# Performance work log

Hardware: AMD Instinct MI355X
Metric: run time of the kernel (lower is better)

## Reference

```python
import jax, jax.numpy as jnp
import numpy as np

NEG_INF = -1e30  # log-semiring zero
B, T, D, V, L = 16, 800, 512, 5000, 100


def setup_inputs() -> dict:
    key = jax.random.key(0)
    k1, k2, k3, k4, k5, k6 = jax.random.split(key, 6)
    hs_pad = jax.random.normal(k1, (B, T, D), dtype=jnp.float32)
    W = jax.random.normal(k2, (D, V), dtype=jnp.float32) / np.sqrt(D)
    b = jnp.zeros((V,), dtype=jnp.float32)
    hlens = jax.random.randint(k3, (B,), T // 2, T + 1, dtype=jnp.int32)
    labels = jax.random.randint(k4, (B, L), 1, V, dtype=jnp.int32)  # blank=0 excluded
    label_lens = jax.random.randint(k5, (B,), L // 2, L + 1, dtype=jnp.int32)
    return {"hs_pad": hs_pad, "W": W, "b": b, "hlens": hlens,
            "labels": labels, "label_lens": label_lens}


def _ctc_tot_scores(log_probs, hlens, labels, label_lens):
    # Standard CTC log-semiring forward DP (equivalent to k2 CTC-topology
    # intersect_dense + get_tot_scores). log_probs: [B,T,V], blank id = 0.
    Bb, Tt, Vv = log_probs.shape
    Ll = labels.shape[1]
    S = 2 * Ll + 1  # extended sequence: blank, l1, blank, l2, ..., blank
    ext = jnp.zeros((Bb, S), dtype=labels.dtype).at[:, 1::2].set(labels)
    # skip transition (s-2 -> s) allowed iff ext[s] != blank and ext[s] != ext[s-2]
    skip = jnp.concatenate(
        [jnp.zeros((Bb, 2), dtype=bool),
         (ext[:, 2:] != ext[:, :-2]) & (ext[:, 2:] != 0)], axis=1)
    # emissions along extended labels: lp_ext[b,t,s] = log_probs[b,t,ext[b,s]]
    lp_ext = jax.vmap(lambda lp, e: lp[:, e])(log_probs, ext)  # [B,T,S]
    alpha = jnp.full((Bb, S), NEG_INF, dtype=log_probs.dtype)
    alpha = alpha.at[:, 0].set(lp_ext[:, 0, 0])
    alpha = alpha.at[:, 1].set(lp_ext[:, 0, 1])

    def step(alpha, inp):
        t, lp_t = inp  # lp_t: [B,S]
        prev1 = jnp.pad(alpha[:, :-1], ((0, 0), (1, 0)), constant_values=NEG_INF)
        prev2 = jnp.pad(alpha[:, :-2], ((0, 0), (2, 0)), constant_values=NEG_INF)
        prev2 = jnp.where(skip, prev2, NEG_INF)
        a = jnp.logaddexp(jnp.logaddexp(alpha, prev1), prev2) + lp_t
        # freeze rows whose sequence has ended (t >= hlen)
        return jnp.where((t < hlens)[:, None], a, alpha), None

    ts = jnp.arange(1, Tt)
    alpha, _ = jax.lax.scan(step, alpha, (ts, jnp.swapaxes(lp_ext, 0, 1)[1:]))
    last = 2 * label_lens  # index of final blank per utterance
    a_last = jnp.take_along_axis(alpha, last[:, None], axis=1)[:, 0]
    a_prev = jnp.take_along_axis(alpha, (last - 1)[:, None], axis=1)[:, 0]
    return jnp.logaddexp(a_last, a_prev)  # [B] total log-likelihoods


def reference(hs_pad, W, b, hlens, labels, label_lens):
    # ctc_lo Linear (dropout_rate=0 -> identity) + log_softmax
    logits = jnp.einsum('btd,dv->btv', hs_pad, W) + b
    log_probs = jax.nn.log_softmax(logits, axis=-1)
    tot = _ctc_tot_scores(log_probs, hlens, labels, label_lens)
    # forward_scores = -tot_scores, reduce=True -> mean
    return jnp.mean(-tot)
```

## Files before the change

### kernel.cpp

```cpp
#include <hip/hip_runtime.h>

#define NEG_INF -1e30f

typedef __attribute__((ext_vector_type(8))) __bf16 bf16x8;
typedef __attribute__((ext_vector_type(4))) float f32x4;

constexpr int Bb = 16, T = 800, D = 512, V = 5000, L = 100;
constexpr int ROWS = Bb * T;
constexpr int S = 2 * L + 1;
constexpr int SP = 208;
constexpr int VP = 5120;
constexpr int NCB = VP / 128;
constexpr int NRB = ROWS / 128;
constexpr int NGB = Bb * 50;
constexpr int CONVB = ROWS * D / 1024;
constexpr int RSTRIDE = SP * 4;
constexpr int CH = 16;
constexpr int CHB = CH * RSTRIDE;

static __device__ __forceinline__ unsigned short f2bf(float x) {
  union { float f; unsigned u; } v; v.f = x;
  unsigned r = (v.u + 0x7FFFu + ((v.u >> 16) & 1u)) >> 16;
  return (unsigned short)r;
}

static __device__ __forceinline__ double dpp_shr1_zero_d(double x) {
  long long b = __double_as_longlong(x);
  int lo = (int)(b & 0xFFFFFFFFLL);
  int hi = (int)(b >> 32);
  int nlo = __builtin_amdgcn_update_dpp(0, lo, 0x138, 0xF, 0xF, false);
  int nhi = __builtin_amdgcn_update_dpp(0, hi, 0x138, 0xF, 0xF, false);
  return __longlong_as_double(((long long)(unsigned)nlo) | ((long long)nhi << 32));
}
static __device__ __forceinline__ double dpp_shl1_zero_d(double x) {
  long long b = __double_as_longlong(x);
  int lo = (int)(b & 0xFFFFFFFFLL);
  int hi = (int)(b >> 32);
  int nlo = __builtin_amdgcn_update_dpp(0, lo, 0x130, 0xF, 0xF, false);
  int nhi = __builtin_amdgcn_update_dpp(0, hi, 0x130, 0xF, 0xF, false);
  return __longlong_as_double(((long long)(unsigned)nlo) | ((long long)nhi << 32));
}
static __device__ __forceinline__ float dpp_shl1_zero_f(float x) {
  return __int_as_float(__builtin_amdgcn_update_dpp(
      0, __float_as_int(x), 0x130, 0xF, 0xF, false));
}

static __device__ __forceinline__ float ex2(float x) { return __builtin_amdgcn_exp2f(x); }
static __device__ __forceinline__ float lg2(float x) { return __builtin_amdgcn_logf(x); }

static __device__ __forceinline__ float lg2d(double z) {
  long long b = __double_as_longlong(z);
  int e = (int)((b >> 52) & 0x7FF);
  if (e == 0) return -1.0e30f;
  unsigned mant = (unsigned)((b >> 29) & 0x7FFFFFu);
  float mf = __int_as_float(0x3F800000u | mant);
  return (float)(e - 1023) + lg2(mf);
}

__global__ __launch_bounds__(256) void k_prep(const float* __restrict__ hs,
                                              const float* __restrict__ W,
                                              unsigned short* __restrict__ A,
                                              unsigned short* __restrict__ Wt) {
  __shared__ float tile[64][65];
  int blk = blockIdx.x;
  if (blk < CONVB) {
    int i = blk * 256 + threadIdx.x;
    float4 f = ((const float4*)hs)[i];
    ushort4 o;
    o.x = f2bf(f.x); o.y = f2bf(f.y); o.z = f2bf(f.z); o.w = f2bf(f.w);
    ((ushort4*)A)[i] = o;
    return;
  }
  int g = blk - CONVB;
  int v0 = (g % (VP / 64)) * 64, k0 = (g / (VP / 64)) * 64;
  int tl = threadIdx.x & 63, th = threadIdx.x >> 6;
#pragma unroll
  for (int i = 0; i < 16; i++) {
    int k = k0 + th + i * 4;
    int v = v0 + tl;
    tile[th + i * 4][tl] = (v < V) ? W[(size_t)k * V + v] : 0.f;
  }
  __syncthreads();
#pragma unroll
  for (int i = 0; i < 16; i++) {
    int v = v0 + th + i * 4;
    int k = k0 + tl;
    Wt[(size_t)v * D + k] = f2bf(tile[tl][th + i * 4]);
  }
}

__global__ __launch_bounds__(256) void k_gather(const unsigned short* __restrict__ A,
                                                const unsigned short* __restrict__ Wt,
                                                const float* __restrict__ bias,
                                                const int* __restrict__ labels,
                                                float* __restrict__ glog) {
  int tid = threadIdx.x;
  int lane = tid & 63, w = tid >> 6;
  int q = lane >> 4, c = lane & 15;
  int b = blockIdx.x & 15, chk = blockIdx.x >> 4;
  int t0 = chk * 16;
  int bT = b * T, bL = b * L;
  int st0 = (w == 0) ? 0 : 4 + (w - 1) * 3;
  int nst = (w == 0) ? 4 : 3;

  int evs[4]; float bvs[4];
#pragma unroll
  for (int j = 0; j < 4; j++) {
    int st = st0 + (j < nst ? j : nst - 1);
    int s = st * 16 + c;
    evs[j] = (s < S && (s & 1)) ? labels[bL + (s >> 1)] : 0;
    bvs[j] = bias[evs[j]];
  }
  const unsigned short* Arow = A + (size_t)(bT + t0 + c) * D;
  f32x4 acc[4];
#pragma unroll
  for (int j = 0; j < 4; j++) acc[j] = (f32x4){0.f, 0.f, 0.f, 0.f};
  for (int kk = 0; kk < D; kk += 32) {
    bf16x8 aa = *(const bf16x8*)(Arow + kk + q * 8);
#pragma unroll
    for (int j = 0; j < 4; j++) {
      bf16x8 bb = *(const bf16x8*)(Wt + (size_t)evs[j] * D + kk + q * 8);
      acc[j] = __builtin_amdgcn_mfma_f32_16x16x32_bf16(aa, bb, acc[j], 0, 0, 0);
    }
  }
#pragma unroll
  for (int j = 0; j < 4; j++) {
    if (j >= nst) break;
    int st = st0 + j;
#pragma unroll
    for (int r = 0; r < 4; r++)
      glog[(size_t)(bT + t0 + q * 4 + r) * SP + st * 16 + c] = acc[j][r] + bvs[j];
  }
}

#define RENORM4(A0, A1, A2, A3, KC) {                                           \
    long long ba0 = __double_as_longlong(A0), ba1 = __double_as_longlong(A1);   \
    long long ba2 = __double_as_longlong(A2), ba3 = __double_as_longlong(A3);   \
    int ee0 = (int)((ba0 >> 52) & 0x7FF), ee1 = (int)((ba1 >> 52) & 0x7FF);     \
    int ee2 = (int)((ba2 >> 52) & 0x7FF), ee3 = (int)((ba3 >> 52) & 0x7FF);     \
    int em = ee0 > ee1 ? ee0 : ee1;                                             \
    em = em > ee2 ? em : ee2;                                                   \
    em = em > ee3 ? em : ee3;                                                   \
    _Pragma("unroll")                                                           \
    for (int o = 1; o < 64; o <<= 1) { int q2 = __shfl_xor(em, o); em = em > q2 ? em : q2; } \
    if (em > 0 && em < 2046) {                                                  \
      double sc = __longlong_as_double((long long)(2046 - em) << 52);           \
      A0 *= sc; A1 *= sc; A2 *= sc; A3 *= sc;                                   \
      KC += em - 1023;                                                          \
    } }

__global__ __launch_bounds__(256) void k_fused(const unsigned short* __restrict__ A,
                                               const unsigned short* __restrict__ Wt,
                                               const float* __restrict__ bias,
                                               const float* __restrict__ glog,
                                               const int* __restrict__ labels,
                                               const int* __restrict__ hlens,
                                               const int* __restrict__ llens,
                                               float* __restrict__ partM,
                                               float* __restrict__ partS,
                                               float* __restrict__ rawtot) {
  __shared__ __attribute__((aligned(16))) char smem[65536];

  int blk = blockIdx.x;
  if (blk < Bb) {
    int tid = threadIdx.x;
    int w = tid >> 6, l = tid & 63;
    if (w >= 2) { __syncthreads(); return; }

    int b = blk;
    int col4 = ((4 * l < SP) ? 4 * l : SP - 4) * 4;
    const char* gvb = (const char*)glog + (size_t)b * T * RSTRIDE;
    int hl = hlens[b];
    int mfw = (hl - 1) >> 1;
    const size_t gmax = (size_t)T * RSTRIDE - 16;

    int i0 = (2 * l < L) ? 2 * l : L - 1;
    int i1 = (2 * l + 1 < L) ? 2 * l + 1 : L - 1;
    int im = (l >= 1) ? 2 * l - 1 : 0; im = im < L ? im : L - 1;
    int lab0 = labels[b * L + i0];
    int lab1 = labels[b * L + i1];
    int labm = labels[b * L + im];
    bool sk1 = (l >= 1) && (lab0 != 0) && (lab0 != labm);
    bool sk3 = (lab1 != 0) && (lab1 != lab0);

    constexpr float LOG2E = 1.44269504f;
    float* laf = (float*)(smem + 53248);
    float* lbf = (float*)(smem + 54080);

    if (w == 0) {
      f32x4 g0 = *(const f32x4*)(gvb + col4);
      double z0 = (l == 0) ? 1.0 : 0.0;
      double z1 = (l == 0) ? (double)ex2((g0.y - g0.x) * LOG2E) : 0.0;
      double z2 = 0.0, z3 = 0.0;
      double Csum = (double)g0.x;
      int Kc = 0;

      auto stageF = [&](int cc, int dst) {
        size_t sb = (size_t)(1 + cc * CH) * RSTRIDE;
#pragma unroll
        for (int pg = 0; pg < 13; pg++) {
          size_t ob = sb + (size_t)pg * 1024 + (size_t)l * 16;
          if (ob > gmax) ob = gmax;
          __builtin_amdgcn_global_load_lds(
              (const __attribute__((address_space(1))) void*)(gvb + ob),
              (__attribute__((address_space(3))) void*)(smem + dst * CHB + pg * 1024),
              16, 0, 0);
        }
      };

#define FW_STEPZ(G) {                                                  \
    float e1f = ex2(((G).y - (G).x) * LOG2E);                          \
    float e3f = ex2(((G).w - (G).x) * LOG2E);                          \
    Csum += (double)(G).x;                                             \
    double p3 = dpp_shr1_zero_d(z3);                                   \
    double nz0 = z0 + p3;                                              \
    double nz1 = (z1 + z0 + (sk1 ? p3 : 0.0)) * (double)e1f;           \
    double nz2 = z2 + z1;                                              \
    double nz3 = (z3 + z2 + (sk3 ? z1 : 0.0)) * (double)e3f;           \
    z0 = nz0; z1 = nz1; z2 = nz2; z3 = nz3; }

      int nchF = (mfw + CH - 1) / CH;
      stageF(0, 0);
      stageF(1, 1);
      for (int c = 0; c < nchF; ++c) {
        int cur = c & 1;
        if (c + 2 < nchF) { asm volatile("s_waitcnt vmcnt(13)" ::: "memory"); }
        else             { asm volatile("s_waitcnt vmcnt(0)" ::: "memory"); }
        __builtin_amdgcn_sched_barrier(0);
        const char* bufc = smem + cur * CHB + col4;
        int steps = mfw - c * CH; if (steps > CH) steps = CH;
        if (steps == CH) {
          f32x4 G[8];
#pragma unroll
          for (int j = 0; j < 8; j++) G[j] = *(const f32x4*)(bufc + j * RSTRIDE);
#pragma unroll
          for (int j = 0; j < 8; j++) FW_STEPZ(G[j])
#pragma unroll
          for (int j = 0; j < 8; j++) G[j] = *(const f32x4*)(bufc + (8 + j) * RSTRIDE);
#pragma unroll
          for (int j = 0; j < 8; j++) FW_STEPZ(G[j])
          RENORM4(z0, z1, z2, z3, Kc)
        } else {
          for (int j = 0; j < steps; j++) {
            f32x4 G = *(const f32x4*)(bufc + j * RSTRIDE);
            FW_STEPZ(G)
          }
        }
        if (c + 2 < nchF) {
          asm volatile("s_waitcnt lgkmcnt(0)" ::: "memory");
          stageF(c + 2, cur);
        }
      }
#undef FW_STEPZ
      if (l < 52) {
        float base = (float)(Csum * 1.4426950408889634 + (double)Kc);
        laf[4 * l + 0] = base + lg2d(z0);
        laf[4 * l + 1] = base + lg2d(z1);
        laf[4 * l + 2] = base + lg2d(z2);
        laf[4 * l + 3] = base + lg2d(z3);
      }
    } else {
      int ll = llens[b];
      int sA = 2 * ll, sB = sA - 1;
      int s0i = 4 * l;
      double b0 = (s0i == sA || s0i == sB) ? 1.0 : 0.0;
      double b1 = (s0i + 1 == sA || s0i + 1 == sB) ? 1.0 : 0.0;
      double b2 = (s0i + 2 == sA || s0i + 2 == sB) ? 1.0 : 0.0;
      double b3 = (s0i + 3 == sA || s0i + 3 == sB) ? 1.0 : 0.0;
      double Csum = 0.0;
      int Kc = 0;
      int sk1i = sk1 ? 1 : 0;
      bool sk1n = __shfl_down(sk1i, 1) != 0;

      auto stageB = [&](int cc, int dst) {
        int rlo = hl - 1 - cc * CH - 15;
        size_t sb = (size_t)rlo * RSTRIDE;
#pragma unroll
        for (int pg = 0; pg < 13; pg++) {
          size_t ob = sb + (size_t)pg * 1024 + (size_t)l * 16;
          if (ob > gmax) ob = gmax;
          __builtin_amdgcn_global_load_lds(
              (const __attribute__((address_space(1))) void*)(gvb + ob),
              (__attribute__((address_space(3))) void*)(smem + dst * CHB + pg * 1024),
              16, 0, 0);
        }
      };

#define BW_STEPZ(G) {                                                  \
    float e1f = ex2(((G).y - (G).x) * LOG2E);                          \
    float e3f = ex2(((G).w - (G).x) * LOG2E);                          \
    float e1s = dpp_shl1_zero_f(e1f);                                  \
    Csum += (double)(G).x;                                             \
    double b1s = dpp_shl1_zero_d(b1);                                  \
    double q4  = dpp_shl1_zero_d(b0);                                  \
    double f1 = b1 * (double)e1f;                                      \
    double f3 = b3 * (double)e3f;                                      \
    double q5 = b1s * (double)e1s;                                     \
    double nb0 = b0 + f1;                                              \
    double nb1 = f1 + b2 + (sk3 ? f3 : 0.0);                           \
    double nb2 = b2 + f3;                                              \
    double nb3 = f3 + q4 + (sk1n ? q5 : 0.0);                          \
    b0 = nb0; b1 = nb1; b2 = nb2; b3 = nb3; }

      int bsteps = (hl - 1) - mfw;
      int nchB = (bsteps + CH - 1) / CH;
      stageB(0, 2);
      stageB(1, 3);
      for (int c = 0; c < nchB; ++c) {
        int cur = c & 1;
        if (c + 2 < nchB) { asm volatile("s_waitcnt vmcnt(13)" ::: "memory"); }
        else             { asm volatile("s_waitcnt vmcnt(0)" ::: "memory"); }
        __builtin_amdgcn_sched_barrier(0);
        const char* bufc = smem + (2 + cur) * CHB + col4;
        int hi = hl - 1 - c * CH;
        int steps = hi - mfw; if (steps > CH) steps = CH;
        if (steps == CH) {
          f32x4 G[8];
#pragma unroll
          for (int j = 0; j < 8; j++) G[j] = *(const f32x4*)(bufc + (15 - j) * RSTRIDE);
#pragma unroll
          for (int j = 0; j < 8; j++) BW_STEPZ(G[j])
#pragma unroll
          for (int j = 0; j < 8; j++) G[j] = *(const f32x4*)(bufc + (7 - j) * RSTRIDE);
#pragma unroll
          for (int j = 0; j < 8; j++) BW_STEPZ(G[j])
          RENORM4(b0, b1, b2, b3, Kc)
        } else {
          for (int j = 0; j < steps; j++) {
            f32x4 G = *(const f32x4*)(bufc + (15 - j) * RSTRIDE);
            BW_STEPZ(G)
          }
        }
        if (c + 2 < nchB) {
          asm volatile("s_waitcnt lgkmcnt(0)" ::: "memory");
          stageB(c + 2, 2 + cur);
        }
      }
#undef BW_STEPZ
      if (l < 52) {
        float base = (float)(Csum * 1.4426950408889634 + (double)Kc);
        lbf[4 * l + 0] = base + lg2d(b0);
        lbf[4 * l + 1] = base + lg2d(b1);
        lbf[4 * l + 2] = base + lg2d(b2);
        lbf[4 * l + 3] = base + lg2d(b3);
      }
    }

    __syncthreads();
    if (w == 0) {
      float v[4];
#pragma unroll
      for (int r = 0; r < 4; r++) {
        int s = 4 * l + r;
        v[r] = (l < 52 && s < S) ? (laf[s] + lbf[s]) : -1.0e30f;
      }
      float mx = fmaxf(fmaxf(v[0], v[1]), fmaxf(v[2], v[3]));
#pragma unroll
      for (int o = 1; o < 64; o <<= 1) mx = fmaxf(mx, __shfl_xor(mx, o));
      float ssum = ex2(v[0] - mx) + ex2(v[1] - mx) + ex2(v[2] - mx) + ex2(v[3] - mx);
#pragma unroll
      for (int o = 1; o < 64; o <<= 1) ssum += __shfl_xor(ssum, o);
      if (l == 0)
        rawtot[b] = 0.6931471805599453f * (mx + lg2(ssum));
    }
    return;
  }

  int gblk = blk - Bb;
  int cb = gblk % NCB, rb = gblk / NCB;
  int tid = threadIdx.x;
  int lane = tid & 63, w = tid >> 6;
  int q = lane >> 4, c = lane & 15;
  int mh = w & 1, nh = w >> 1;
  int row0 = rb * 128, n0 = cb * 128;
  int lr = lane >> 3, lc = lane & 7;
  int oc = (lc ^ lr) * 8;

  auto stageG = [&](int bufsel, int kk) {
#pragma unroll
    for (int j = 0; j < 4; j++) {
      int i = w * 4 + j;
      const unsigned short* ga = A + (size_t)(row0 + i * 8 + lr) * D + kk + oc;
      __builtin_amdgcn_global_load_lds(
          (const __attribute__((address_space(1))) void*)ga,
          (__attribute__((address_space(3))) void*)(smem + bufsel * 16384 + i * 1024),
          16, 0, 0);
      const unsigned short* gb = Wt + (size_t)(n0 + i * 8 + lr) * D + kk + oc;
      __builtin_amdgcn_global_load_lds(
          (const __attribute__((address_space(1))) void*)gb,
          (__attribute__((address_space(3))) void*)(smem + 32768 + bufsel * 16384 + i * 1024),
          16, 0, 0);
    }
  };

  f32x4 acc[4][4];
#pragma unroll
  for (int mt = 0; mt < 4; mt++)
#pragma unroll
    for (int nt = 0; nt < 4; nt++) acc[mt][nt] = (f32x4){0.f, 0.f, 0.f, 0.f};

  stageG(0, 0);
  __syncthreads();
  int cur = 0;
  for (int kt = 0; kt < 8; kt++) {
    if (kt + 1 < 8) stageG(cur ^ 1, (kt + 1) * 64);
    const unsigned short* Ab = (const unsigned short*)(smem + cur * 16384);
    const unsigned short* Bb2 = (const unsigned short*)(smem + 32768 + cur * 16384);
#pragma unroll
    for (int kq = 0; kq < 2; kq++) {
      int o = ((kq * 4 + q) ^ (c & 7)) * 8;
      bf16x8 af[4], bfr[4];
#pragma unroll
      for (int mt = 0; mt < 4; mt++)
        af[mt] = *(const bf16x8*)(Ab + (mh * 64 + mt * 16 + c) * 64 + o);
#pragma unroll
      for (int nt = 0; nt < 4; nt++)
        bfr[nt] = *(const bf16x8*)(Bb2 + (nh * 64 + nt * 16 + c) * 64 + o);
#pragma unroll
      for (int mt = 0; mt < 4; mt++)
#pragma unroll
        for (int nt = 0; nt < 4; nt++)
          acc[mt][nt] = __builtin_amdgcn_mfma_f32_16x16x32_bf16(af[mt], bfr[nt], acc[mt][nt], 0, 0, 0);
    }
    __syncthreads();
    cur ^= 1;
  }

  float (*redM)[128] = (float (*)[128])(smem + 0);
  float (*redS)[128] = (float (*)[128])(smem + 1024);

  int vcb[4]; float bv[4];
#pragma unroll
  for (int nt = 0; nt < 4; nt++) {
    vcb[nt] = n0 + nh * 64 + nt * 16 + c;
    bv[nt] = (vcb[nt] < V) ? bias[vcb[nt]] : 0.f;
  }
#pragma unroll
  for (int mt = 0; mt < 4; mt++) {
#pragma unroll
    for (int r = 0; r < 4; r++) {
      float x[4]; float m = NEG_INF;
#pragma unroll
      for (int nt = 0; nt < 4; nt++) {
        x[nt] = (vcb[nt] < V) ? (acc[mt][nt][r] + bv[nt]) : NEG_INF;
        m = fmaxf(m, x[nt]);
      }
#pragma unroll
      for (int o = 1; o < 16; o <<= 1) m = fmaxf(m, __shfl_xor(m, o));
      float s = 0.f;
#pragma unroll
      for (int nt = 0; nt < 4; nt++) s += __expf(x[nt] - m);
#pragma unroll
      for (int o = 1; o < 16; o <<= 1) s += __shfl_xor(s, o);
      if (c == 0) {
        int rloc = mh * 64 + mt * 16 + q * 4 + r;
        redM[nh][rloc] = m;
        redS[nh][rloc] = s;
      }
    }
  }
  __syncthreads();
  if (tid < 128) {
    float m0 = redM[0][tid], m1 = redM[1][tid];
    float mm = fmaxf(m0, m1);
    float ss = redS[0][tid] * __expf(m0 - mm) + redS[1][tid] * __expf(m1 - mm);
    partM[(size_t)cb * ROWS + row0 + tid] = mm;
    partS[(size_t)cb * ROWS + row0 + tid] = ss;
  }
}

__global__ __launch_bounds__(256) void k_lse(const float* __restrict__ pM,
                                             const float* __restrict__ pS,
                                             float* __restrict__ lse) {
  int row = blockIdx.x * 256 + threadIdx.x;
  float m = pM[row], s = pS[row];
  for (int cb = 1; cb < NCB; cb++) {
    float M2 = pM[(size_t)cb * ROWS + row], S2 = pS[(size_t)cb * ROWS + row];
    float mn = fmaxf(m, M2);
    s = s * __expf(m - mn) + S2 * __expf(M2 - mn);
    m = mn;
  }
  lse[row] = m + __logf(s);
}

__global__ __launch_bounds__(1024) void k_final(const float* __restrict__ lse,
                                                const float* __restrict__ rawtot,
                                                const int* __restrict__ hlens,
                                                float* __restrict__ out) {
  __shared__ float acc[Bb];
  int w = threadIdx.x >> 6, l = threadIdx.x & 63;
  int hl = hlens[w];
  float s = 0.f;
  for (int t = l; t < hl; t += 64) s += lse[w * T + t];
#pragma unroll
  for (int o = 1; o < 64; o <<= 1) s += __shfl_xor(s, o);
  if (l == 0) acc[w] = rawtot[w] - s;
  __syncthreads();
  if (threadIdx.x == 0) {
    float m = 0.f;
    for (int i = 0; i < Bb; i++) m += acc[i];
    out[0] = -m / (float)Bb;
  }
}

extern "C" void kernel_launch(void* const* d_in, const int* in_sizes, int n_in,
                              void* d_out, int out_size, void* d_ws, size_t ws_size,
                              hipStream_t stream) {
  const float* hs    = (const float*)d_in[0];
  const float* W     = (const float*)d_in[1];
  const float* bias  = (const float*)d_in[2];
  const int* hlens   = (const int*)d_in[3];
  const int* labels  = (const int*)d_in[4];
  const int* llens   = (const int*)d_in[5];
  float* out = (float*)d_out;

  char* ws = (char*)d_ws;
  unsigned short* A    = (unsigned short*)(ws);
  unsigned short* Wt   = (unsigned short*)(ws + 13107200);
  float*          partM= (float*)(ws + 18350080);
  float*          partS= (float*)(ws + 20398080);
  float*          lse  = (float*)(ws + 22446080);
  float*          glog = (float*)(ws + 22497280);
  float*          rawtot=(float*)(ws + 33146880);

  k_prep<<<CONVB + (VP / 64) * (D / 64), 256, 0, stream>>>(hs, W, A, Wt);
  k_gather<<<NGB, 256, 0, stream>>>(A, Wt, bias, labels, glog);
  k_fused<<<Bb + NCB * NRB, 256, 0, stream>>>(A, Wt, bias, glog, labels, hlens, llens,
                                              partM, partS, rawtot);
  k_lse<<<ROWS / 256, 256, 0, stream>>>(partM, partS, lse);
  k_final<<<1, 1024, 0, stream>>>(lse, rawtot, hlens, out);

  (void)in_sizes; (void)n_in; (void)out_size; (void)ws_size;
}
```

Measured before the change: 241.6 us.

## Fuse label-logit gather GEMM into CTC DP blocks with producer warps

Removes the separate k_gather launch and its global glog buffer. In each DP block, warps 2 and 3 now compute the gathered label logits for 16-timestep chunks with MFMA straight into LDS, while warps 0 and 1 run the forward and backward recurrences on the previous chunk, double-buffered with __syncthreads. This drops one kernel launch and a global write/read round trip. In exchange, the serial DP critical path now waits each chunk on a 13-tile MFMA producer and a block barrier, and renormalization now runs every chunk.

```diff
diff --git a/kernel.cpp b/kernel.cpp
--- a/kernel.cpp
+++ b/kernel.cpp
@@ -12,7 +12,6 @@
 constexpr int VP = 5120;
 constexpr int NCB = VP / 128;
 constexpr int NRB = ROWS / 128;
-constexpr int NGB = Bb * 50;
 constexpr int CONVB = ROWS * D / 1024;
 constexpr int RSTRIDE = SP * 4;
 constexpr int CH = 16;
@@ -86,50 +85,6 @@
     int v = v0 + th + i * 4;
     int k = k0 + tl;
     Wt[(size_t)v * D + k] = f2bf(tile[tl][th + i * 4]);
-  }
-}
-
-__global__ __launch_bounds__(256) void k_gather(const unsigned short* __restrict__ A,
-                                                const unsigned short* __restrict__ Wt,
-                                                const float* __restrict__ bias,
-                                                const int* __restrict__ labels,
-                                                float* __restrict__ glog) {
-  int tid = threadIdx.x;
-  int lane = tid & 63, w = tid >> 6;
-  int q = lane >> 4, c = lane & 15;
-  int b = blockIdx.x & 15, chk = blockIdx.x >> 4;
-  int t0 = chk * 16;
-  int bT = b * T, bL = b * L;
-  int st0 = (w == 0) ? 0 : 4 + (w - 1) * 3;
-  int nst = (w == 0) ? 4 : 3;
-
-  int evs[4]; float bvs[4];
-#pragma unroll
-  for (int j = 0; j < 4; j++) {
-    int st = st0 + (j < nst ? j : nst - 1);
-    int s = st * 16 + c;
-    evs[j] = (s < S && (s & 1)) ? labels[bL + (s >> 1)] : 0;
-    bvs[j] = bias[evs[j]];
-  }
-  const unsigned short* Arow = A + (size_t)(bT + t0 + c) * D;
-  f32x4 acc[4];
-#pragma unroll
-  for (int j = 0; j < 4; j++) acc[j] = (f32x4){0.f, 0.f, 0.f, 0.f};
-  for (int kk = 0; kk < D; kk += 32) {
-    bf16x8 aa = *(const bf16x8*)(Arow + kk + q * 8);
-#pragma unroll
-    for (int j = 0; j < 4; j++) {
-      bf16x8 bb = *(const bf16x8*)(Wt + (size_t)evs[j] * D + kk + q * 8);
-      acc[j] = __builtin_amdgcn_mfma_f32_16x16x32_bf16(aa, bb, acc[j], 0, 0, 0);
-    }
-  }
-#pragma unroll
-  for (int j = 0; j < 4; j++) {
-    if (j >= nst) break;
-    int st = st0 + j;
-#pragma unroll
-    for (int r = 0; r < 4; r++)
-      glog[(size_t)(bT + t0 + q * 4 + r) * SP + st * 16 + c] = acc[j][r] + bvs[j];
   }
 }
 
@@ -152,7 +107,6 @@
 __global__ __launch_bounds__(256) void k_fused(const unsigned short* __restrict__ A,
                                                const unsigned short* __restrict__ Wt,
                                                const float* __restrict__ bias,
-                                               const float* __restrict__ glog,
                                                const int* __restrict__ labels,
                                                const int* __restrict__ hlens,
                                                const int* __restrict__ llens,
@@ -165,53 +119,99 @@
   if (blk < Bb) {
     int tid = threadIdx.x;
     int w = tid >> 6, l = tid & 63;
-    if (w >= 2) { __syncthreads(); return; }
-
+    int c16 = l & 15, q = l >> 4;
     int b = blk;
     int col4 = ((4 * l < SP) ? 4 * l : SP - 4) * 4;
-    const char* gvb = (const char*)glog + (size_t)b * T * RSTRIDE;
     int hl = hlens[b];
     int mfw = (hl - 1) >> 1;
-    const size_t gmax = (size_t)T * RSTRIDE - 16;
+    int bsteps = (hl - 1) - mfw;
+    int nchF = mfw / 16 + 1;
+    int nchB = (bsteps + 15) / 16;
+    int nmax = nchF > nchB ? nchF : nchB;
+    int bT = b * T, bL = b * L;
+    constexpr float LOG2E = 1.44269504f;
+    float* laf = (float*)(smem + 53248);
+    float* lbf = (float*)(smem + 54080);
 
     int i0 = (2 * l < L) ? 2 * l : L - 1;
     int i1 = (2 * l + 1 < L) ? 2 * l + 1 : L - 1;
     int im = (l >= 1) ? 2 * l - 1 : 0; im = im < L ? im : L - 1;
-    int lab0 = labels[b * L + i0];
-    int lab1 = labels[b * L + i1];
-    int labm = labels[b * L + im];
+    int lab0 = labels[bL + i0];
+    int lab1 = labels[bL + i1];
+    int labm = labels[bL + im];
     bool sk1 = (l >= 1) && (lab0 != 0) && (lab0 != labm);
     bool sk3 = (lab1 != 0) && (lab1 != lab0);
-
-    constexpr float LOG2E = 1.44269504f;
-    float* laf = (float*)(smem + 53248);
-    float* lbf = (float*)(smem + 54080);
-
-    if (w == 0) {
-      f32x4 g0 = *(const f32x4*)(gvb + col4);
-      double z0 = (l == 0) ? 1.0 : 0.0;
-      double z1 = (l == 0) ? (double)ex2((g0.y - g0.x) * LOG2E) : 0.0;
-      double z2 = 0.0, z3 = 0.0;
-      double Csum = (double)g0.x;
-      int Kc = 0;
-
-      auto stageF = [&](int cc, int dst) {
-        size_t sb = (size_t)(1 + cc * CH) * RSTRIDE;
-#pragma unroll
-        for (int pg = 0; pg < 13; pg++) {
-          size_t ob = sb + (size_t)pg * 1024 + (size_t)l * 16;
-          if (ob > gmax) ob = gmax;
-          __builtin_amdgcn_global_load_lds(
-              (const __attribute__((address_space(1))) void*)(gvb + ob),
-              (__attribute__((address_space(3))) void*)(smem + dst * CHB + pg * 1024),
-              16, 0, 0);
+    int sk1i = sk1 ? 1 : 0;
+    bool sk1n = __shfl_down(sk1i, 1) != 0;
+
+    int evs[13]; float bvs[13];
+    if (w >= 2) {
+#pragma unroll
+      for (int st = 0; st < 13; st++) {
+        int s = st * 16 + c16;
+        evs[st] = (s < S && (s & 1)) ? labels[bL + (s >> 1)] : 0;
+        bvs[st] = bias[evs[st]];
+      }
+    }
+
+    auto produce = [&](int t0, char* dst) {
+      const unsigned short* Arow = A + (size_t)(bT + t0 + c16) * D;
+      {
+        f32x4 acc[7];
+#pragma unroll
+        for (int j = 0; j < 7; j++) acc[j] = (f32x4){0.f, 0.f, 0.f, 0.f};
+        for (int kk = 0; kk < D; kk += 32) {
+          bf16x8 aa = *(const bf16x8*)(Arow + kk + q * 8);
+#pragma unroll
+          for (int j = 0; j < 7; j++) {
+            bf16x8 bb = *(const bf16x8*)(Wt + (size_t)evs[j] * D + kk + q * 8);
+            acc[j] = __builtin_amdgcn_mfma_f32_16x16x32_bf16(aa, bb, acc[j], 0, 0, 0);
+          }
         }
-      };
+#pragma unroll
+        for (int j = 0; j < 7; j++)
+#pragma unroll
+          for (int r = 0; r < 4; r++)
+            *(float*)(dst + (q * 4 + r) * RSTRIDE + (j * 16 + c16) * 4) = acc[j][r] + bvs[j];
+      }
+      {
+        f32x4 acc[6];
+#pragma unroll
+        for (int j = 0; j < 6; j++) acc[j] = (f32x4){0.f, 0.f, 0.f, 0.f};
+        for (int kk = 0; kk < D; kk += 32) {
+          bf16x8 aa = *(const bf16x8*)(Arow + kk + q * 8);
+#pragma unroll
+          for (int j = 0; j < 6; j++) {
+            bf16x8 bb = *(const bf16x8*)(Wt + (size_t)evs[7 + j] * D + kk + q * 8);
+            acc[j] = __builtin_amdgcn_mfma_f32_16x16x32_bf16(aa, bb, acc[j], 0, 0, 0);
+          }
+        }
+#pragma unroll
+        for (int j = 0; j < 6; j++)
+#pragma unroll
+          for (int r = 0; r < 4; r++)
+            *(float*)(dst + (q * 4 + r) * RSTRIDE + ((7 + j) * 16 + c16) * 4) = acc[j][r] + bvs[7 + j];
+      }
+    };
+
+    double z0 = 0.0, z1 = 0.0, z2 = 0.0, z3 = 0.0;
+    double bb0 = 0.0, bb1 = 0.0, bb2 = 0.0, bb3 = 0.0;
+    double CsumF = 0.0, CsumB = 0.0;
+    int KcF = 0, KcB = 0;
+    if (w == 1) {
+      int ll = llens[b];
+      int sA = 2 * ll, sB = sA - 1;
+      int s0i = 4 * l;
+      bb0 = (s0i == sA || s0i == sB) ? 1.0 : 0.0;
+      bb1 = (s0i + 1 == sA || s0i + 1 == sB) ? 1.0 : 0.0;
+      bb2 = (s0i + 2 == sA || s0i + 2 == sB) ? 1.0 : 0.0;
+      bb3 = (s0i + 3 == sA || s0i + 3 == sB) ? 1.0 : 0.0;
+    }
 
 #define FW_STEPZ(G) {                                                  \
     float e1f = ex2(((G).y - (G).x) * LOG2E);                          \
     float e3f = ex2(((G).w - (G).x) * LOG2E);                          \
-    Csum += (double)(G).x;                                             \
+    CsumF += (double)(G).x;                                            \
     double p3 = dpp_shr1_zero_d(z3);                                   \
     double nz0 = z0 + p3;                                              \
     double nz1 = (z1 + z0 + (sk1 ? p3 : 0.0)) * (double)e1f;           \
@@ -219,133 +219,84 @@
     double nz3 = (z3 + z2 + (sk3 ? z1 : 0.0)) * (double)e3f;           \
     z0 = nz0; z1 = nz1; z2 = nz2; z3 = nz3; }
 
-      int nchF = (mfw + CH - 1) / CH;
-      stageF(0, 0);
-      stageF(1, 1);
-      for (int c = 0; c < nchF; ++c) {
-        int cur = c & 1;
-        if (c + 2 < nchF) { asm volatile("s_waitcnt vmcnt(13)" ::: "memory"); }
-        else             { asm volatile("s_waitcnt vmcnt(0)" ::: "memory"); }
-        __builtin_amdgcn_sched_barrier(0);
-        const char* bufc = smem + cur * CHB + col4;
-        int steps = mfw - c * CH; if (steps > CH) steps = CH;
-        if (steps == CH) {
-          f32x4 G[8];
-#pragma unroll
-          for (int j = 0; j < 8; j++) G[j] = *(const f32x4*)(bufc + j * RSTRIDE);
-#pragma unroll
-          for (int j = 0; j < 8; j++) FW_STEPZ(G[j])
-#pragma unroll
-          for (int j = 0; j < 8; j++) G[j] = *(const f32x4*)(bufc + (8 + j) * RSTRIDE);
-#pragma unroll
-          for (int j = 0; j < 8; j++) FW_STEPZ(G[j])
-          RENORM4(z0, z1, z2, z3, Kc)
-        } else {
-          for (int j = 0; j < steps; j++) {
-            f32x4 G = *(const f32x4*)(bufc + j * RSTRIDE);
-            FW_STEPZ(G)
-          }
-        }
-        if (c + 2 < nchF) {
-          asm volatile("s_waitcnt lgkmcnt(0)" ::: "memory");
-          stageF(c + 2, cur);
-        }
-      }
-#undef FW_STEPZ
-      if (l < 52) {
-        float base = (float)(Csum * 1.4426950408889634 + (double)Kc);
-        laf[4 * l + 0] = base + lg2d(z0);
-        laf[4 * l + 1] = base + lg2d(z1);
-        laf[4 * l + 2] = base + lg2d(z2);
-        laf[4 * l + 3] = base + lg2d(z3);
-      }
-    } else {
-      int ll = llens[b];
-      int sA = 2 * ll, sB = sA - 1;
-      int s0i = 4 * l;
-      double b0 = (s0i == sA || s0i == sB) ? 1.0 : 0.0;
-      double b1 = (s0i + 1 == sA || s0i + 1 == sB) ? 1.0 : 0.0;
-      double b2 = (s0i + 2 == sA || s0i + 2 == sB) ? 1.0 : 0.0;
-      double b3 = (s0i + 3 == sA || s0i + 3 == sB) ? 1.0 : 0.0;
-      double Csum = 0.0;
-      int Kc = 0;
-      int sk1i = sk1 ? 1 : 0;
-      bool sk1n = __shfl_down(sk1i, 1) != 0;
-
-      auto stageB = [&](int cc, int dst) {
-        int rlo = hl - 1 - cc * CH - 15;
-        size_t sb = (size_t)rlo * RSTRIDE;
-#pragma unroll
-        for (int pg = 0; pg < 13; pg++) {
-          size_t ob = sb + (size_t)pg * 1024 + (size_t)l * 16;
-          if (ob > gmax) ob = gmax;
-          __builtin_amdgcn_global_load_lds(
-              (const __attribute__((address_space(1))) void*)(gvb + ob),
-              (__attribute__((address_space(3))) void*)(smem + dst * CHB + pg * 1024),
-              16, 0, 0);
-        }
-      };
-
 #define BW_STEPZ(G) {                                                  \
     float e1f = ex2(((G).y - (G).x) * LOG2E);                          \
     float e3f = ex2(((G).w - (G).x) * LOG2E);                          \
     float e1s = dpp_shl1_zero_f(e1f);                                  \
-    Csum += (double)(G).x;                                             \
-    double b1s = dpp_shl1_zero_d(b1);                                  \
-    double q4  = dpp_shl1_zero_d(b0);                                  \
-    double f1 = b1 * (double)e1f;                                      \
-    double f3 = b3 * (double)e3f;                                      \
+    CsumB += (double)(G).x;                                            \
+    double b1s = dpp_shl1_zero_d(bb1);                                 \
+    double q4  = dpp_shl1_zero_d(bb0);                                 \
+    double f1 = bb1 * (double)e1f;                                     \
+    double f3 = bb3 * (double)e3f;                                     \
     double q5 = b1s * (double)e1s;                                     \
-    double nb0 = b0 + f1;                                              \
-    double nb1 = f1 + b2 + (sk3 ? f3 : 0.0);                           \
-    double nb2 = b2 + f3;                                              \
+    double nb0 = bb0 + f1;                                             \
+    double nb1 = f1 + bb2 + (sk3 ? f3 : 0.0);                          \
+    double nb2 = bb2 + f3;                                             \
     double nb3 = f3 + q4 + (sk1n ? q5 : 0.0);                          \
-    b0 = nb0; b1 = nb1; b2 = nb2; b3 = nb3; }
-
-      int bsteps = (hl - 1) - mfw;
-      int nchB = (bsteps + CH - 1) / CH;
-      stageB(0, 2);
-      stageB(1, 3);
-      for (int c = 0; c < nchB; ++c) {
-        int cur = c & 1;
-        if (c + 2 < nchB) { asm volatile("s_waitcnt vmcnt(13)" ::: "memory"); }
-        else             { asm volatile("s_waitcnt vmcnt(0)" ::: "memory"); }
-        __builtin_amdgcn_sched_barrier(0);
-        const char* bufc = smem + (2 + cur) * CHB + col4;
-        int hi = hl - 1 - c * CH;
-        int steps = hi - mfw; if (steps > CH) steps = CH;
-        if (steps == CH) {
-          f32x4 G[8];
-#pragma unroll
-          for (int j = 0; j < 8; j++) G[j] = *(const f32x4*)(bufc + (15 - j) * RSTRIDE);
-#pragma unroll
-          for (int j = 0; j < 8; j++) BW_STEPZ(G[j])
-#pragma unroll
-          for (int j = 0; j < 8; j++) G[j] = *(const f32x4*)(bufc + (7 - j) * RSTRIDE);
-#pragma unroll
-          for (int j = 0; j < 8; j++) BW_STEPZ(G[j])
-          RENORM4(b0, b1, b2, b3, Kc)
-        } else {
-          for (int j = 0; j < steps; j++) {
-            f32x4 G = *(const f32x4*)(bufc + (15 - j) * RSTRIDE);
+    bb0 = nb0; bb1 = nb1; bb2 = nb2; bb3 = nb3; }
+
+    if (w == 2) produce(0, smem);
+    if (w == 3) produce(hl - 16, smem + 2 * CHB);
+    __syncthreads();
+
+    for (int cc = 0; cc < nmax; ++cc) {
+      if (w == 0) {
+        if (cc < nchF) {
+          const char* bufc = smem + (cc & 1) * CHB + col4;
+          if (cc == 0) {
+            f32x4 g0 = *(const f32x4*)bufc;
+            z0 = (l == 0) ? 1.0 : 0.0;
+            z1 = (l == 0) ? (double)ex2((g0.y - g0.x) * LOG2E) : 0.0;
+            z2 = 0.0; z3 = 0.0;
+            CsumF = (double)g0.x;
+            for (int j = 1; j < 16; j++) {
+              f32x4 G = *(const f32x4*)(bufc + j * RSTRIDE);
+              FW_STEPZ(G)
+            }
+          } else {
+            int tb = cc * 16;
+            int steps = mfw - tb + 1; if (steps > 16) steps = 16;
+            for (int j = 0; j < steps; j++) {
+              f32x4 G = *(const f32x4*)(bufc + j * RSTRIDE);
+              FW_STEPZ(G)
+            }
+          }
+          RENORM4(z0, z1, z2, z3, KcF)
+        }
+      } else if (w == 1) {
+        if (cc < nchB) {
+          const char* bufc = smem + (2 + (cc & 1)) * CHB + col4;
+          int steps = bsteps - cc * 16; if (steps > 16) steps = 16;
+          for (int jj = 0; jj < steps; jj++) {
+            f32x4 G = *(const f32x4*)(bufc + (15 - jj) * RSTRIDE);
             BW_STEPZ(G)
           }
+          RENORM4(bb0, bb1, bb2, bb3, KcB)
         }
-        if (c + 2 < nchB) {
-          asm volatile("s_waitcnt lgkmcnt(0)" ::: "memory");
-          stageB(c + 2, 2 + cur);
-        }
-      }
+      } else if (w == 2) {
+        if (cc + 1 < nchF) produce((cc + 1) * 16, smem + ((cc + 1) & 1) * CHB);
+      } else {
+        if (cc + 1 < nchB) produce(hl - 16 - 16 * (cc + 1), smem + (2 + ((cc + 1) & 1)) * CHB);
+      }
+      __syncthreads();
+    }
+#undef FW_STEPZ
 #undef BW_STEPZ
-      if (l < 52) {
-        float base = (float)(Csum * 1.4426950408889634 + (double)Kc);
-        lbf[4 * l + 0] = base + lg2d(b0);
-        lbf[4 * l + 1] = base + lg2d(b1);
-        lbf[4 * l + 2] = base + lg2d(b2);
-        lbf[4 * l + 3] = base + lg2d(b3);
-      }
-    }
-
+
+    if (w == 0 && l < 52) {
+      float base = (float)(CsumF * 1.4426950408889634 + (double)KcF);
+      laf[4 * l + 0] = base + lg2d(z0);
+      laf[4 * l + 1] = base + lg2d(z1);
+      laf[4 * l + 2] = base + lg2d(z2);
+      laf[4 * l + 3] = base + lg2d(z3);
+    }
+    if (w == 1 && l < 52) {
+      float base = (float)(CsumB * 1.4426950408889634 + (double)KcB);
+      lbf[4 * l + 0] = base + lg2d(bb0);
+      lbf[4 * l + 1] = base + lg2d(bb1);
+      lbf[4 * l + 2] = base + lg2d(bb2);
+      lbf[4 * l + 3] = base + lg2d(bb3);
+    }
     __syncthreads();
     if (w == 0) {
       float v[4];
@@ -520,12 +471,10 @@
   float*          partM= (float*)(ws + 18350080);
   float*          partS= (float*)(ws + 20398080);
   float*          lse  = (float*)(ws + 22446080);
-  float*          glog = (float*)(ws + 22497280);
-  float*          rawtot=(float*)(ws + 33146880);
+  float*          rawtot=(float*)(ws + 22497280);
 
   k_prep<<<CONVB + (VP / 64) * (D / 64), 256, 0, stream>>>(hs, W, A, Wt);
-  k_gather<<<NGB, 256, 0, stream>>>(A, Wt, bias, labels, glog);
-  k_fused<<<Bb + NCB * NRB, 256, 0, stream>>>(A, Wt, bias, glog, labels, hlens, llens,
+  k_fused<<<Bb + NCB * NRB, 256, 0, stream>>>(A, Wt, bias, labels, hlens, llens,
                                               partM, partS, rawtot);
   k_lse<<<ROWS / 256, 256, 0, stream>>>(partM, partS, lse);
   k_final<<<1, 1024, 0, stream>>>(lse, rawtot, hlens, out);
```

Result: slower. 395.9 us (+63.9%).
